# Performance work log

Hardware: AMD Instinct MI355X
Metric: run time of the kernel (lower is better)

## Reference

```python
import jax, jax.numpy as jnp
import numpy as np

DIM = 1024
HEADS = 16
HEAD_DIM = DIM // HEADS
SCALE = HEAD_DIM ** -0.5


def setup_inputs() -> dict:
    key = jax.random.key(0)
    k1, k2, k3, k4 = jax.random.split(key, 4)
    x = jax.random.normal(k1, (2, 2048, DIM), dtype=jnp.float32)
    # nn.Linear(dim, 3*dim, bias=False): weight shape (3*dim, dim), y = x @ W.T
    w_qkv = jax.random.normal(k2, (3 * DIM, DIM), dtype=jnp.float32) * (DIM ** -0.5)
    w_proj = jax.random.normal(k3, (DIM, DIM), dtype=jnp.float32) * (DIM ** -0.5)
    head_w = jnp.ones((HEADS,), dtype=jnp.float32)
    return {"x": x, "w_qkv": w_qkv, "w_proj": w_proj, "head_w": head_w}


def reference(x, w_qkv, w_proj, head_w) -> jnp.ndarray:
    B, N, C = x.shape
    qkv = jnp.einsum("bnc,dc->bnd", x, w_qkv)  # [B,N,3C]
    qkv = qkv.reshape(B, N, 3, HEADS, HEAD_DIM).transpose(2, 0, 3, 1, 4)
    q, k, v = qkv[0], qkv[1], qkv[2]  # each [B,H,N,Dh]
    attn = jnp.einsum("bhqd,bhkd->bhqk", q, k) * SCALE  # [B,H,N,N]
    attn = jax.nn.softmax(attn, axis=-1)
    out = jnp.einsum("bhqk,bhkd->bhqd", attn, v)  # [B,H,N,Dh]
    hw = jax.nn.softmax(head_w)[None, :, None, None]
    out = out * hw
    out = out.transpose(0, 2, 1, 3).reshape(B, N, C)
    return jnp.einsum("bnc,dc->bnd", out, w_proj)
```

## Files before the change

kernel.cpp:

```cpp
#include <hip/hip_runtime.h>

typedef _Float16 half_t;
typedef _Float16 half8 __attribute__((ext_vector_type(8)));
typedef _Float16 half4_t __attribute__((ext_vector_type(4)));
typedef float floatx4 __attribute__((ext_vector_type(4)));

#define B_SZ 2
#define SEQ 2048
#define DIM_ 1024
#define NH 16
#define DH 64
#define ROWS (B_SZ * SEQ)

__device__ __forceinline__ void gl2lds16(const void* g, void* l) {
  __builtin_amdgcn_global_load_lds((const __attribute__((address_space(1))) unsigned int*)g,
                                   (__attribute__((address_space(3))) unsigned int*)l, 16, 0, 0);
}

__global__ void convert_f32_f16(const float4* __restrict__ src, half4_t* __restrict__ dst, int n4) {
  int i = blockIdx.x * blockDim.x + threadIdx.x;
  if (i < n4) {
    float4 v = src[i];
    half4_t h;
    h.x = (half_t)v.x; h.y = (half_t)v.y; h.z = (half_t)v.z; h.w = (half_t)v.w;
    dst[i] = h;
  }
}

template <int MODE>
__global__ __launch_bounds__(256) void gemm128(const half_t* __restrict__ A,
                                               const half_t* __restrict__ Bt,
                                               half_t* __restrict__ q16,
                                               half_t* __restrict__ k16,
                                               half_t* __restrict__ vT16,
                                               float* __restrict__ outp) {
  constexpr int K = 1024;
  __shared__ __align__(16) half_t a_lds[128 * 32];
  __shared__ __align__(16) half_t b_lds[128 * 32];
  const int t = threadIdx.x;
  const int wave = t >> 6, lane = t & 63;
  const int l15 = lane & 15, quad = lane >> 4;
  const int wm = wave >> 1, wn = wave & 1;
  const int row0 = blockIdx.y * 128, col0 = blockIdx.x * 128;

  floatx4 acc[4][4];
  const floatx4 z4 = {0.f, 0.f, 0.f, 0.f};
#pragma unroll
  for (int i = 0; i < 4; ++i)
#pragma unroll
    for (int j = 0; j < 4; ++j) acc[i][j] = z4;

  for (int k0 = 0; k0 < K; k0 += 32) {
#pragma unroll
    for (int hi = 0; hi < 2; ++hi) {
      int s = t + hi * 256;
      int row = s >> 2, c = s & 3;
      int sc = c ^ ((row >> 1) & 3);
      gl2lds16(A + (size_t)(row0 + row) * K + (k0 + sc * 8), a_lds + (wave * 64 + hi * 256) * 8);
      gl2lds16(Bt + (size_t)(col0 + row) * K + (k0 + sc * 8), b_lds + (wave * 64 + hi * 256) * 8);
    }
    __syncthreads();
    half8 af[4], bf[4];
#pragma unroll
    for (int mt = 0; mt < 4; ++mt) {
      int row = wm * 64 + mt * 16 + l15;
      af[mt] = *(const half8*)(a_lds + row * 32 + (quad ^ ((row >> 1) & 3)) * 8);
    }
#pragma unroll
    for (int nt = 0; nt < 4; ++nt) {
      int row = wn * 64 + nt * 16 + l15;
      bf[nt] = *(const half8*)(b_lds + row * 32 + (quad ^ ((row >> 1) & 3)) * 8);
    }
#pragma unroll
    for (int mt = 0; mt < 4; ++mt)
#pragma unroll
      for (int nt = 0; nt < 4; ++nt)
        acc[mt][nt] = __builtin_amdgcn_mfma_f32_16x16x32_f16(af[mt], bf[nt], acc[mt][nt], 0, 0, 0);
    __syncthreads();
  }

  if (MODE == 0) {
    const int which = col0 >> 10;
#pragma unroll
    for (int mt = 0; mt < 4; ++mt)
#pragma unroll
      for (int nt = 0; nt < 4; ++nt) {
        int rbase = row0 + wm * 64 + mt * 16 + quad * 4;
        int gcol = col0 + wn * 64 + nt * 16 + l15;
        int hc = gcol & 1023, h = hc >> 6, d = hc & 63;
#pragma unroll
        for (int r = 0; r < 4; ++r) {
          int grow = rbase + r;
          int b = grow >> 11, n = grow & 2047;
          int bh = b * NH + h;
          float v = acc[mt][nt][r];
          if (which == 0)
            q16[((size_t)bh * SEQ + n) * DH + d] = (half_t)(v * 0.125f);
          else if (which == 1)
            k16[((size_t)bh * SEQ + n) * DH + d] = (half_t)v;
          else
            vT16[((size_t)bh * DH + d) * SEQ + n] = (half_t)v;
        }
      }
  } else {
#pragma unroll
    for (int mt = 0; mt < 4; ++mt)
#pragma unroll
      for (int nt = 0; nt < 4; ++nt) {
        int rbase = row0 + wm * 64 + mt * 16 + quad * 4;
        int gcol = col0 + wn * 64 + nt * 16 + l15;
#pragma unroll
        for (int r = 0; r < 4; ++r)
          outp[(size_t)(rbase + r) * DIM_ + gcol] = acc[mt][nt][r];
      }
  }
}

__global__ __launch_bounds__(256) void attn_fa(const half_t* __restrict__ q16,
                                               const half_t* __restrict__ k16,
                                               const half_t* __restrict__ vT16,
                                               const float* __restrict__ head_w,
                                               half_t* __restrict__ attn16) {
  __shared__ __align__(16) half_t k_lds[2][64 * 64];
  __shared__ __align__(16) half_t v_lds[2][64 * 64];
  __shared__ __align__(16) half_t p_lds[4][512];

  const int t = threadIdx.x;
  const int wave = t >> 6, lane = t & 63;
  const int l15 = lane & 15, quad = lane >> 4;
  const int bh = blockIdx.x >> 5, qt = blockIdx.x & 31;
  const int h = bh & 15, b = bh >> 4;
  const half_t* qp = q16 + (size_t)bh * SEQ * DH;
  const half_t* kp = k16 + (size_t)bh * SEQ * DH;
  const half_t* vp = vT16 + (size_t)bh * DH * SEQ;
  const int q0 = qt * 64 + wave * 16;

  const int s0 = t, s1 = t + 256;
  const int r0_ = s0 >> 3, c0_ = (s0 & 7) ^ (r0_ & 7);
  const int r1_ = s1 >> 3, c1_ = (s1 & 7) ^ (r1_ & 7);

  half8 qf[2];
#pragma unroll
  for (int kf = 0; kf < 2; ++kf)
    qf[kf] = *(const half8*)(qp + (size_t)(q0 + l15) * DH + kf * 32 + quad * 8);

  const floatx4 z4 = {0.f, 0.f, 0.f, 0.f};
  floatx4 o[4];
  float psum[4];
#pragma unroll
  for (int i = 0; i < 4; ++i) { o[i] = z4; psum[i] = 0.f; }

  half_t* pw = p_lds[wave];

  {
    const int j0 = 0;
    gl2lds16(kp + (size_t)(j0 + r0_) * DH + c0_ * 8, &k_lds[0][(wave * 64) * 8]);
    gl2lds16(vp + (size_t)r0_ * SEQ + j0 + c0_ * 8, &v_lds[0][(wave * 64) * 8]);
    gl2lds16(kp + (size_t)(j0 + r1_) * DH + c1_ * 8, &k_lds[0][(wave * 64 + 256) * 8]);
    gl2lds16(vp + (size_t)r1_ * SEQ + j0 + c1_ * 8, &v_lds[0][(wave * 64 + 256) * 8]);
  }

  int cur = 0;
  for (int jt = 0; jt < 32; ++jt) {
    __syncthreads();

    if (jt + 1 < 32) {
      const int j0 = (jt + 1) * 64, nb = cur ^ 1;
      gl2lds16(kp + (size_t)(j0 + r0_) * DH + c0_ * 8, &k_lds[nb][(wave * 64) * 8]);
      gl2lds16(vp + (size_t)r0_ * SEQ + j0 + c0_ * 8, &v_lds[nb][(wave * 64) * 8]);
      gl2lds16(kp + (size_t)(j0 + r1_) * DH + c1_ * 8, &k_lds[nb][(wave * 64 + 256) * 8]);
      gl2lds16(vp + (size_t)r1_ * SEQ + j0 + c1_ * 8, &v_lds[nb][(wave * 64 + 256) * 8]);
    }

    const half_t* kl = k_lds[cur];
    const half_t* vl = v_lds[cur];

    floatx4 sacc[4];
#pragma unroll
    for (int nt = 0; nt < 4; ++nt) sacc[nt] = z4;
#pragma unroll
    for (int kf = 0; kf < 2; ++kf)
#pragma unroll
      for (int nt = 0; nt < 4; ++nt) {
        int row = nt * 16 + l15;
        half8 kb = *(const half8*)(kl + row * 64 + (((kf << 2) | quad) ^ (row & 7)) * 8);
        sacc[nt] = __builtin_amdgcn_mfma_f32_16x16x32_f16(qf[kf], kb, sacc[nt], 0, 0, 0);
      }

    float p[4][4];
#pragma unroll
    for (int nt = 0; nt < 4; ++nt)
#pragma unroll
      for (int r = 0; r < 4; ++r) p[nt][r] = __expf(sacc[nt][r]);
#pragma unroll
    for (int r = 0; r < 4; ++r) psum[r] += p[0][r] + p[1][r] + p[2][r] + p[3][r];

#pragma unroll
    for (int kf = 0; kf < 2; ++kf) {
#pragma unroll
      for (int nt2 = 0; nt2 < 2; ++nt2) {
        int nt = kf * 2 + nt2;
#pragma unroll
        for (int r = 0; r < 4; ++r) {
          int row = quad * 4 + r, col = nt2 * 16 + l15;
          pw[((col >> 3) * 16 + row) * 8 + (col & 7)] = (half_t)p[nt][r];
        }
      }
      half8 pf = *(const half8*)(pw + (quad * 16 + l15) * 8);
#pragma unroll
      for (int nt = 0; nt < 4; ++nt) {
        int vrow = nt * 16 + l15;
        half8 vb = *(const half8*)(vl + vrow * 64 + (((kf << 2) | quad) ^ (vrow & 7)) * 8);
        o[nt] = __builtin_amdgcn_mfma_f32_16x16x32_f16(pf, vb, o[nt], 0, 0, 0);
      }
    }
    cur ^= 1;
  }

#pragma unroll
  for (int r = 0; r < 4; ++r) {
#pragma unroll
    for (int dm = 1; dm < 16; dm <<= 1) psum[r] += __shfl_xor(psum[r], dm, 64);
  }

  float mw = head_w[0];
#pragma unroll
  for (int i = 1; i < NH; ++i) mw = fmaxf(mw, head_w[i]);
  float sw = 0.f;
#pragma unroll
  for (int i = 0; i < NH; ++i) sw += __expf(head_w[i] - mw);
  float hwv = __expf(head_w[h] - mw) / sw;

#pragma unroll
  for (int r = 0; r < 4; ++r) {
    float scl = hwv / psum[r];
    int n = q0 + quad * 4 + r;
#pragma unroll
    for (int nt = 0; nt < 4; ++nt) {
      int col = h * DH + nt * 16 + l15;
      attn16[((size_t)(b * SEQ + n)) * DIM_ + col] = (half_t)(o[nt][r] * scl);
    }
  }
}

extern "C" void kernel_launch(void* const* d_in, const int* in_sizes, int n_in,
                              void* d_out, int out_size, void* d_ws, size_t ws_size,
                              hipStream_t stream) {
  const float* x = (const float*)d_in[0];
  const float* w_qkv = (const float*)d_in[1];
  const float* w_proj = (const float*)d_in[2];
  const float* head_w = (const float*)d_in[3];
  float* out = (float*)d_out;

  half_t* x16 = (half_t*)d_ws;
  half_t* wq16 = x16 + (size_t)ROWS * DIM_;
  half_t* wp16 = wq16 + (size_t)3 * DIM_ * DIM_;
  half_t* q16 = wp16 + (size_t)DIM_ * DIM_;
  half_t* k16 = q16 + (size_t)ROWS * DIM_;
  half_t* vT16 = k16 + (size_t)ROWS * DIM_;
  half_t* attn16 = vT16 + (size_t)ROWS * DIM_;

  convert_f32_f16<<<ROWS * DIM_ / 4 / 256, 256, 0, stream>>>((const float4*)x, (half4_t*)x16,
                                                             ROWS * DIM_ / 4);
  convert_f32_f16<<<3 * DIM_ * DIM_ / 4 / 256, 256, 0, stream>>>((const float4*)w_qkv,
                                                                 (half4_t*)wq16, 3 * DIM_ * DIM_ / 4);
  convert_f32_f16<<<DIM_ * DIM_ / 4 / 256, 256, 0, stream>>>((const float4*)w_proj, (half4_t*)wp16,
                                                             DIM_ * DIM_ / 4);

  gemm128<0><<<dim3(24, 32), 256, 0, stream>>>(x16, wq16, q16, k16, vT16, nullptr);
  attn_fa<<<B_SZ * NH * (SEQ / 64), 256, 0, stream>>>(q16, k16, vT16, head_w, attn16);
  gemm128<1><<<dim3(8, 32), 256, 0, stream>>>(attn16, wp16, nullptr, nullptr, nullptr, out);
}
```

Measured before the change: 218.7 us.

## Process two query tiles per wave in attention, fuse conversions, vectorize V stores

The attention kernel now gives each wave 32 query rows instead of 16, so every K/V fragment read from LDS feeds two MFMAs. This halves the grid and the K/V global traffic per query, and it stores P through a swizzled 64-wide LDS buffer. The three f32-to-f16 conversion kernels are merged into one launch. The transposed V epilogue writes half4 vectors instead of scalar stores. The attention change raises register and LDS use and cuts the block count to 512, which may lower occupancy.

```diff
diff --git a/kernel.cpp b/kernel.cpp
--- a/kernel.cpp
+++ b/kernel.cpp
@@ -17,14 +17,18 @@
                                    (__attribute__((address_space(3))) unsigned int*)l, 16, 0, 0);
 }
 
-__global__ void convert_f32_f16(const float4* __restrict__ src, half4_t* __restrict__ dst, int n4) {
+__global__ void convert_all(const float4* __restrict__ x, const float4* __restrict__ wq,
+                            const float4* __restrict__ wp, half4_t* __restrict__ dst,
+                            int nx, int nq, int np) {
   int i = blockIdx.x * blockDim.x + threadIdx.x;
-  if (i < n4) {
-    float4 v = src[i];
-    half4_t h;
-    h.x = (half_t)v.x; h.y = (half_t)v.y; h.z = (half_t)v.z; h.w = (half_t)v.w;
-    dst[i] = h;
-  }
+  float4 v;
+  if (i < nx) v = x[i];
+  else if (i < nx + nq) v = wq[i - nx];
+  else if (i < nx + nq + np) v = wp[i - nx - nq];
+  else return;
+  half4_t h;
+  h.x = (half_t)v.x; h.y = (half_t)v.y; h.z = (half_t)v.z; h.w = (half_t)v.w;
+  dst[i] = h;
 }
 
 template <int MODE>
@@ -88,18 +92,24 @@
         int rbase = row0 + wm * 64 + mt * 16 + quad * 4;
         int gcol = col0 + wn * 64 + nt * 16 + l15;
         int hc = gcol & 1023, h = hc >> 6, d = hc & 63;
-#pragma unroll
-        for (int r = 0; r < 4; ++r) {
-          int grow = rbase + r;
-          int b = grow >> 11, n = grow & 2047;
-          int bh = b * NH + h;
-          float v = acc[mt][nt][r];
-          if (which == 0)
-            q16[((size_t)bh * SEQ + n) * DH + d] = (half_t)(v * 0.125f);
-          else if (which == 1)
-            k16[((size_t)bh * SEQ + n) * DH + d] = (half_t)v;
-          else
-            vT16[((size_t)bh * DH + d) * SEQ + n] = (half_t)v;
+        int b = rbase >> 11, n0 = rbase & 2047;
+        int bh = b * NH + h;
+        if (which == 2) {
+          half4_t h4;
+          h4.x = (half_t)acc[mt][nt][0];
+          h4.y = (half_t)acc[mt][nt][1];
+          h4.z = (half_t)acc[mt][nt][2];
+          h4.w = (half_t)acc[mt][nt][3];
+          *(half4_t*)(vT16 + ((size_t)bh * DH + d) * SEQ + n0) = h4;
+        } else {
+#pragma unroll
+          for (int r = 0; r < 4; ++r) {
+            float v = acc[mt][nt][r];
+            if (which == 0)
+              q16[((size_t)bh * SEQ + n0 + r) * DH + d] = (half_t)(v * 0.125f);
+            else
+              k16[((size_t)bh * SEQ + n0 + r) * DH + d] = (half_t)v;
+          }
         }
       }
   } else {
@@ -123,42 +133,44 @@
                                                half_t* __restrict__ attn16) {
   __shared__ __align__(16) half_t k_lds[2][64 * 64];
   __shared__ __align__(16) half_t v_lds[2][64 * 64];
-  __shared__ __align__(16) half_t p_lds[4][512];
+  __shared__ __align__(16) half_t p_lds[8 * 1024];
 
   const int t = threadIdx.x;
   const int wave = t >> 6, lane = t & 63;
   const int l15 = lane & 15, quad = lane >> 4;
-  const int bh = blockIdx.x >> 5, qt = blockIdx.x & 31;
+  const int bh = blockIdx.x >> 4, qt = blockIdx.x & 15;
   const int h = bh & 15, b = bh >> 4;
   const half_t* qp = q16 + (size_t)bh * SEQ * DH;
   const half_t* kp = k16 + (size_t)bh * SEQ * DH;
   const half_t* vp = vT16 + (size_t)bh * DH * SEQ;
-  const int q0 = qt * 64 + wave * 16;
+  const int q0w = qt * 128 + wave * 32;
 
   const int s0 = t, s1 = t + 256;
   const int r0_ = s0 >> 3, c0_ = (s0 & 7) ^ (r0_ & 7);
   const int r1_ = s1 >> 3, c1_ = (s1 & 7) ^ (r1_ & 7);
 
-  half8 qf[2];
-#pragma unroll
-  for (int kf = 0; kf < 2; ++kf)
-    qf[kf] = *(const half8*)(qp + (size_t)(q0 + l15) * DH + kf * 32 + quad * 8);
+  half8 qf[2][2];
+#pragma unroll
+  for (int mi = 0; mi < 2; ++mi)
+#pragma unroll
+    for (int kf = 0; kf < 2; ++kf)
+      qf[mi][kf] = *(const half8*)(qp + (size_t)(q0w + mi * 16 + l15) * DH + kf * 32 + quad * 8);
 
   const floatx4 z4 = {0.f, 0.f, 0.f, 0.f};
-  floatx4 o[4];
-  float psum[4];
-#pragma unroll
-  for (int i = 0; i < 4; ++i) { o[i] = z4; psum[i] = 0.f; }
-
-  half_t* pw = p_lds[wave];
-
-  {
-    const int j0 = 0;
-    gl2lds16(kp + (size_t)(j0 + r0_) * DH + c0_ * 8, &k_lds[0][(wave * 64) * 8]);
-    gl2lds16(vp + (size_t)r0_ * SEQ + j0 + c0_ * 8, &v_lds[0][(wave * 64) * 8]);
-    gl2lds16(kp + (size_t)(j0 + r1_) * DH + c1_ * 8, &k_lds[0][(wave * 64 + 256) * 8]);
-    gl2lds16(vp + (size_t)r1_ * SEQ + j0 + c1_ * 8, &v_lds[0][(wave * 64 + 256) * 8]);
-  }
+  floatx4 o[2][4];
+  float psum[2][4];
+#pragma unroll
+  for (int mi = 0; mi < 2; ++mi)
+#pragma unroll
+    for (int i = 0; i < 4; ++i) { o[mi][i] = z4; psum[mi][i] = 0.f; }
+
+  const int prow = quad * 4;
+  const int rswz = (l15 + (l15 >> 3)) & 7;
+
+  gl2lds16(kp + (size_t)r0_ * DH + c0_ * 8, &k_lds[0][(wave * 64) * 8]);
+  gl2lds16(vp + (size_t)r0_ * SEQ + c0_ * 8, &v_lds[0][(wave * 64) * 8]);
+  gl2lds16(kp + (size_t)r1_ * DH + c1_ * 8, &k_lds[0][(wave * 64 + 256) * 8]);
+  gl2lds16(vp + (size_t)r1_ * SEQ + c1_ * 8, &v_lds[0][(wave * 64 + 256) * 8]);
 
   int cur = 0;
   for (int jt = 0; jt < 32; ++jt) {
@@ -175,53 +187,60 @@
     const half_t* kl = k_lds[cur];
     const half_t* vl = v_lds[cur];
 
-    floatx4 sacc[4];
-#pragma unroll
-    for (int nt = 0; nt < 4; ++nt) sacc[nt] = z4;
+    floatx4 sacc[2][4];
+#pragma unroll
+    for (int mi = 0; mi < 2; ++mi)
+#pragma unroll
+      for (int nt = 0; nt < 4; ++nt) sacc[mi][nt] = z4;
 #pragma unroll
     for (int kf = 0; kf < 2; ++kf)
 #pragma unroll
       for (int nt = 0; nt < 4; ++nt) {
         int row = nt * 16 + l15;
         half8 kb = *(const half8*)(kl + row * 64 + (((kf << 2) | quad) ^ (row & 7)) * 8);
-        sacc[nt] = __builtin_amdgcn_mfma_f32_16x16x32_f16(qf[kf], kb, sacc[nt], 0, 0, 0);
-      }
-
-    float p[4][4];
-#pragma unroll
-    for (int nt = 0; nt < 4; ++nt)
-#pragma unroll
-      for (int r = 0; r < 4; ++r) p[nt][r] = __expf(sacc[nt][r]);
-#pragma unroll
-    for (int r = 0; r < 4; ++r) psum[r] += p[0][r] + p[1][r] + p[2][r] + p[3][r];
+        sacc[0][nt] = __builtin_amdgcn_mfma_f32_16x16x32_f16(qf[0][kf], kb, sacc[0][nt], 0, 0, 0);
+        sacc[1][nt] = __builtin_amdgcn_mfma_f32_16x16x32_f16(qf[1][kf], kb, sacc[1][nt], 0, 0, 0);
+      }
+
+#pragma unroll
+    for (int mi = 0; mi < 2; ++mi) {
+      half_t* pw = p_lds + (wave * 2 + mi) * 1024;
+#pragma unroll
+      for (int nt = 0; nt < 4; ++nt)
+#pragma unroll
+        for (int r = 0; r < 4; ++r) {
+          float p = __expf(sacc[mi][nt][r]);
+          psum[mi][r] += p;
+          int row = prow + r, col = nt * 16 + l15;
+          int swz = (row + (row >> 3)) & 7;
+          pw[row * 64 + (((col >> 3) ^ swz) << 3) + (col & 7)] = (half_t)p;
+        }
+    }
 
 #pragma unroll
     for (int kf = 0; kf < 2; ++kf) {
-#pragma unroll
-      for (int nt2 = 0; nt2 < 2; ++nt2) {
-        int nt = kf * 2 + nt2;
-#pragma unroll
-        for (int r = 0; r < 4; ++r) {
-          int row = quad * 4 + r, col = nt2 * 16 + l15;
-          pw[((col >> 3) * 16 + row) * 8 + (col & 7)] = (half_t)p[nt][r];
-        }
-      }
-      half8 pf = *(const half8*)(pw + (quad * 16 + l15) * 8);
+      half8 pf0 = *(const half8*)(p_lds + (wave * 2 + 0) * 1024 + l15 * 64 +
+                                  ((((kf << 2) | quad) ^ rswz) << 3));
+      half8 pf1 = *(const half8*)(p_lds + (wave * 2 + 1) * 1024 + l15 * 64 +
+                                  ((((kf << 2) | quad) ^ rswz) << 3));
 #pragma unroll
       for (int nt = 0; nt < 4; ++nt) {
         int vrow = nt * 16 + l15;
         half8 vb = *(const half8*)(vl + vrow * 64 + (((kf << 2) | quad) ^ (vrow & 7)) * 8);
-        o[nt] = __builtin_amdgcn_mfma_f32_16x16x32_f16(pf, vb, o[nt], 0, 0, 0);
+        o[0][nt] = __builtin_amdgcn_mfma_f32_16x16x32_f16(pf0, vb, o[0][nt], 0, 0, 0);
+        o[1][nt] = __builtin_amdgcn_mfma_f32_16x16x32_f16(pf1, vb, o[1][nt], 0, 0, 0);
       }
     }
     cur ^= 1;
   }
 
 #pragma unroll
-  for (int r = 0; r < 4; ++r) {
-#pragma unroll
-    for (int dm = 1; dm < 16; dm <<= 1) psum[r] += __shfl_xor(psum[r], dm, 64);
-  }
+  for (int mi = 0; mi < 2; ++mi)
+#pragma unroll
+    for (int r = 0; r < 4; ++r) {
+#pragma unroll
+      for (int dm = 1; dm < 16; dm <<= 1) psum[mi][r] += __shfl_xor(psum[mi][r], dm, 64);
+    }
 
   float mw = head_w[0];
 #pragma unroll
@@ -232,15 +251,17 @@
   float hwv = __expf(head_w[h] - mw) / sw;
 
 #pragma unroll
-  for (int r = 0; r < 4; ++r) {
-    float scl = hwv / psum[r];
-    int n = q0 + quad * 4 + r;
-#pragma unroll
-    for (int nt = 0; nt < 4; ++nt) {
-      int col = h * DH + nt * 16 + l15;
-      attn16[((size_t)(b * SEQ + n)) * DIM_ + col] = (half_t)(o[nt][r] * scl);
-    }
-  }
+  for (int mi = 0; mi < 2; ++mi)
+#pragma unroll
+    for (int r = 0; r < 4; ++r) {
+      float scl = hwv / psum[mi][r];
+      int n = q0w + mi * 16 + quad * 4 + r;
+#pragma unroll
+      for (int nt = 0; nt < 4; ++nt) {
+        int col = h * DH + nt * 16 + l15;
+        attn16[((size_t)(b * SEQ + n)) * DIM_ + col] = (half_t)(o[mi][nt][r] * scl);
+      }
+    }
 }
 
 extern "C" void kernel_launch(void* const* d_in, const int* in_sizes, int n_in,
@@ -260,14 +281,12 @@
   half_t* vT16 = k16 + (size_t)ROWS * DIM_;
   half_t* attn16 = vT16 + (size_t)ROWS * DIM_;
 
-  convert_f32_f16<<<ROWS * DIM_ / 4 / 256, 256, 0, stream>>>((const float4*)x, (half4_t*)x16,
-                                                             ROWS * DIM_ / 4);
-  convert_f32_f16<<<3 * DIM_ * DIM_ / 4 / 256, 256, 0, stream>>>((const float4*)w_qkv,
-                                                                 (half4_t*)wq16, 3 * DIM_ * DIM_ / 4);
-  convert_f32_f16<<<DIM_ * DIM_ / 4 / 256, 256, 0, stream>>>((const float4*)w_proj, (half4_t*)wp16,
-                                                             DIM_ * DIM_ / 4);
+  const int nx = ROWS * DIM_ / 4, nq = 3 * DIM_ * DIM_ / 4, np = DIM_ * DIM_ / 4;
+  convert_all<<<(nx + nq + np) / 256, 256, 0, stream>>>((const float4*)x, (const float4*)w_qkv,
+                                                        (const float4*)w_proj, (half4_t*)x16,
+                                                        nx, nq, np);
 
   gemm128<0><<<dim3(24, 32), 256, 0, stream>>>(x16, wq16, q16, k16, vT16, nullptr);
-  attn_fa<<<B_SZ * NH * (SEQ / 64), 256, 0, stream>>>(q16, k16, vT16, head_w, attn16);
+  attn_fa<<<B_SZ * NH * (SEQ / 128), 256, 0, stream>>>(q16, k16, vT16, head_w, attn16);
   gemm128<1><<<dim3(8, 32), 256, 0, stream>>>(attn16, wp16, nullptr, nullptr, nullptr, out);
 }
```

Result: faster. 207.4 us (-5.2%).
